# Optimization experiments

Measured on AMD Instinct MI355X. Metric: run time of the kernel, lower is better.

The kernel has to match this reference:

```python
import jax, jax.numpy as jnp
import numpy as np

B, V, D, H = 8192, 5, 1792, 14
HD = D // H  # head dim = 128
NEG = jnp.float32(-1e30)  # stand-in for -inf in the adjacency mask


def setup_inputs() -> dict:
    key = jax.random.key(0)
    ks = jax.random.split(key, 5)
    vertices = jax.random.normal(ks[0], (B, V, D), dtype=jnp.float32)
    adjacency = jax.random.randint(ks[1], (V, V), 0, 2, dtype=jnp.int32)
    # ensure no all-masked row (self connection), matching a valid pentachoron graph
    adjacency = adjacency.at[jnp.arange(V), jnp.arange(V)].set(1)
    scale = 1.0 / np.sqrt(D)
    in_proj_w = jax.random.normal(ks[2], (3 * D, D), dtype=jnp.float32) * scale
    in_proj_b = jnp.zeros((3 * D,), dtype=jnp.float32)
    out_proj_w = jax.random.normal(ks[3], (D, D), dtype=jnp.float32) * scale
    out_proj_b = jnp.zeros((D,), dtype=jnp.float32)
    return {"vertices": vertices, "adjacency": adjacency,
            "in_proj_w": in_proj_w, "in_proj_b": in_proj_b,
            "out_proj_w": out_proj_w, "out_proj_b": out_proj_b}


def reference(vertices, adjacency, in_proj_w, in_proj_b, out_proj_w, out_proj_b):
    # Fused equivalent of looping MultiheadAttention over the 5 vertices:
    # query i attends over all 5 vertices, masked by adjacency row i.
    qkv = jnp.einsum('bvd,ed->bve', vertices, in_proj_w) + in_proj_b  # [B,V,3D]
    q, k, v = jnp.split(qkv, 3, axis=-1)
    # [B,H,V,HD]
    q = q.reshape(B, V, H, HD).transpose(0, 2, 1, 3)
    k = k.reshape(B, V, H, HD).transpose(0, 2, 1, 3)
    v = v.reshape(B, V, H, HD).transpose(0, 2, 1, 3)
    scores = jnp.einsum('bhqd,bhkd->bhqk', q, k) / jnp.float32(np.sqrt(HD))
    mask = jnp.where(adjacency == 0, NEG, jnp.float32(0.0))  # [V,V]
    scores = scores + mask[None, None, :, :]
    attn = jax.nn.softmax(scores, axis=-1)
    out = jnp.einsum('bhqk,bhkd->bhqd', attn, v)  # [B,H,V,HD]
    out = out.transpose(0, 2, 1, 3).reshape(B, V, D)
    return jnp.einsum('bvd,ed->bve', out, out_proj_w) + out_proj_b
```

## Files before the change

kernel.cpp:

```cpp
#include <hip/hip_runtime.h>
#include <hip/hip_bf16.h>

#define Bsz   8192
#define Vn    5
#define Dm    1792
#define Hn    14
#define HDm   128
#define Mrows (Bsz * Vn)
#define N1    (3 * Dm)
#define Kd    Dm

typedef float f32x4 __attribute__((ext_vector_type(4)));
typedef short bf16x8 __attribute__((ext_vector_type(8)));

__device__ __forceinline__ ushort f2bf(float f) {
    unsigned u = __float_as_uint(f);
    u += 0x7fffu + ((u >> 16) & 1u);
    return (ushort)(u >> 16);
}
__device__ __forceinline__ float bf2f(ushort h) {
    return __uint_as_float(((unsigned)h) << 16);
}

#define AS1(p) ((const __attribute__((address_space(1))) void*)(p))
#define AS3(p) ((__attribute__((address_space(3))) void*)(p))

__global__ void cvt_kernel(const float* __restrict__ in, ushort* __restrict__ out, int n4) {
    int i = blockIdx.x * blockDim.x + threadIdx.x;
    int stride = gridDim.x * blockDim.x;
    for (int idx = i; idx < n4; idx += stride) {
        float4 v = reinterpret_cast<const float4*>(in)[idx];
        ushort4 o;
        o.x = f2bf(v.x); o.y = f2bf(v.y); o.z = f2bf(v.z); o.w = f2bf(v.w);
        reinterpret_cast<ushort4*>(out)[idx] = o;
    }
}

template<bool OUT_BF16>
__global__ __launch_bounds__(512, 2) void gemm8p(
    const ushort* __restrict__ A,
    const ushort* __restrict__ Bw,
    const float* __restrict__ bias,
    void* __restrict__ Cout,
    int M, int N, int K)
{
    __shared__ __align__(16) char smem[131072];

    const int nTN = N >> 8;
    int bid = blockIdx.x;
    int cpx = gridDim.x >> 3;
    int swz = (bid & 7) * cpx + (bid >> 3);
    int gsz = 4 * nTN;
    int g = swz / gsz, r = swz - g * gsz;
    int bm = g * 4 + (r & 3);
    int bn = r >> 2;

    int t = threadIdx.x;
    int lane = t & 63, w = t >> 6;
    int wrow = (w >> 2) * 128;
    int wcol = (w & 3) * 64;
    int fr = lane & 15, fq = lane >> 4;
    int slotC = ((fq ^ ((fr >> 1) & 3)) << 4);
    int aOff = (wrow + fr) * 64 + slotC;
    int bOff = 32768 + (wcol + fr) * 64 + slotC;

    size_t K2 = (size_t)K * 2;
    size_t rowSkip = (size_t)128 * K2;
    int rowL = t >> 2;
    int slotSw = (((t & 3) ^ ((t >> 3) & 3)) << 4);
    const char* aSrc = (const char*)A + (size_t)(bm * 256 + rowL) * K2 + slotSw;
    const char* bSrc = (const char*)Bw + (size_t)(bn * 256 + rowL) * K2 + slotSw;

    f32x4 acc[8][4] = {};
    bf16x8 af0[4], af1[4], bf0[4], bf1[4];

#define STAGE(SRC, UOFF, KT, KH) { \
    const char* _s = (SRC) + (size_t)(KT) * 128 + (KH) * 64; \
    __builtin_amdgcn_global_load_lds(AS1(_s), AS3(&smem[(UOFF) + t * 16]), 16, 0, 0); \
    __builtin_amdgcn_global_load_lds(AS1(_s + rowSkip), AS3(&smem[(UOFF) + 8192 + t * 16]), 16, 0, 0); }

#define RDA(DST, BUF, KS, M0) { \
    DST[0] = *(const bf16x8*)&smem[(BUF)*65536 + (KS)*16384 + ((M0)+0)*1024 + aOff]; \
    DST[1] = *(const bf16x8*)&smem[(BUF)*65536 + (KS)*16384 + ((M0)+1)*1024 + aOff]; \
    DST[2] = *(const bf16x8*)&smem[(BUF)*65536 + (KS)*16384 + ((M0)+2)*1024 + aOff]; \
    DST[3] = *(const bf16x8*)&smem[(BUF)*65536 + (KS)*16384 + ((M0)+3)*1024 + aOff]; }

#define RDB(DST, BUF, KS) { \
    DST[0] = *(const bf16x8*)&smem[(BUF)*65536 + (KS)*16384 + 0*1024 + bOff]; \
    DST[1] = *(const bf16x8*)&smem[(BUF)*65536 + (KS)*16384 + 1*1024 + bOff]; \
    DST[2] = *(const bf16x8*)&smem[(BUF)*65536 + (KS)*16384 + 2*1024 + bOff]; \
    DST[3] = *(const bf16x8*)&smem[(BUF)*65536 + (KS)*16384 + 3*1024 + bOff]; }

#define MFMAQ(AF, BF, M0) { \
    __builtin_amdgcn_s_setprio(1); \
    _Pragma("unroll") \
    for (int mi = 0; mi < 4; ++mi) { \
      _Pragma("unroll") \
      for (int ni = 0; ni < 4; ++ni) \
        acc[(M0)+mi][ni] = __builtin_amdgcn_mfma_f32_16x16x32_bf16(AF[mi], BF[ni], acc[(M0)+mi][ni], 0, 0, 0); \
    } \
    __builtin_amdgcn_s_setprio(0); }

#define BAR __builtin_amdgcn_s_barrier()
#define VMC(N) asm volatile("s_waitcnt vmcnt(" #N ")" ::: "memory")

    STAGE(aSrc, 0,      0, 0);
    STAGE(bSrc, 32768,  0, 0);
    STAGE(aSrc, 16384,  0, 1);
    STAGE(bSrc, 49152,  0, 1);
    STAGE(aSrc, 65536,  1, 0);
    STAGE(bSrc, 98304,  1, 0);
    VMC(8);
    BAR;
    RDA(af0, 0, 0, 0); RDB(bf0, 0, 0);

    const int NIT = K / 128;
    #pragma unroll 1
    for (int it = 0; it < NIT - 1; ++it) {
        int kt1 = 2 * it + 1, kt2 = 2 * it + 2, kt3 = 2 * it + 3;
        MFMAQ(af0, bf0, 0); RDA(af1, 0, 0, 4);                 STAGE(aSrc, 81920, kt1, 1);
        VMC(6); BAR;
        MFMAQ(af1, bf0, 4); RDA(af0, 0, 1, 0); RDB(bf1, 0, 1); STAGE(bSrc, 114688, kt1, 1);
        BAR;
        MFMAQ(af0, bf1, 0); RDA(af1, 0, 1, 4);                 STAGE(aSrc, 0, kt2, 0);
        VMC(6); BAR;
        MFMAQ(af1, bf1, 4); RDA(af0, 1, 0, 0); RDB(bf0, 1, 0); STAGE(bSrc, 32768, kt2, 0);
        BAR;
        MFMAQ(af0, bf0, 0); RDA(af1, 1, 0, 4);                 STAGE(aSrc, 16384, kt2, 1);
        VMC(6); BAR;
        MFMAQ(af1, bf0, 4); RDA(af0, 1, 1, 0); RDB(bf1, 1, 1); STAGE(bSrc, 49152, kt2, 1);
        BAR;
        MFMAQ(af0, bf1, 0); RDA(af1, 1, 1, 4);                 STAGE(aSrc, 65536, kt3, 0);
        VMC(6); BAR;
        MFMAQ(af1, bf1, 4); RDA(af0, 0, 0, 0); RDB(bf0, 0, 0); STAGE(bSrc, 98304, kt3, 0);
        BAR;
    }
    {
        int kt1 = 2 * NIT - 1;
        MFMAQ(af0, bf0, 0); RDA(af1, 0, 0, 4);                 STAGE(aSrc, 81920, kt1, 1);
        VMC(6); BAR;
        MFMAQ(af1, bf0, 4); RDA(af0, 0, 1, 0); RDB(bf1, 0, 1); STAGE(bSrc, 114688, kt1, 1);
        BAR;
        MFMAQ(af0, bf1, 0); RDA(af1, 0, 1, 4);
        VMC(4); BAR;
        MFMAQ(af1, bf1, 4); RDA(af0, 1, 0, 0); RDB(bf0, 1, 0);
        BAR;
        MFMAQ(af0, bf0, 0); RDA(af1, 1, 0, 4);
        VMC(0); BAR;
        MFMAQ(af1, bf0, 4); RDA(af0, 1, 1, 0); RDB(bf1, 1, 1);
        BAR;
        MFMAQ(af0, bf1, 0); RDA(af1, 1, 1, 4);
        BAR;
        MFMAQ(af1, bf1, 4);
    }

#undef STAGE
#undef RDA
#undef RDB
#undef MFMAQ
#undef BAR
#undef VMC

    float*  Cf = (float*)Cout;
    ushort* Cb = (ushort*)Cout;
    #pragma unroll
    for (int mi = 0; mi < 8; ++mi) {
        int row0 = bm * 256 + wrow + mi * 16 + fq * 4;
        #pragma unroll
        for (int ni = 0; ni < 4; ++ni) {
            int col = bn * 256 + wcol + ni * 16 + fr;
            float bv = bias[col];
            #pragma unroll
            for (int rr = 0; rr < 4; ++rr) {
                float val = acc[mi][ni][rr] + bv;
                size_t off = (size_t)(row0 + rr) * N + col;
                if (OUT_BF16) Cb[off] = f2bf(val);
                else          Cf[off] = val;
            }
        }
    }
}

__global__ __launch_bounds__(256) void attn_kernel(
    const ushort* __restrict__ qkv,
    const int* __restrict__ adj,
    ushort* __restrict__ outp)
{
    int gw = blockIdx.x * 4 + (threadIdx.x >> 6);
    int lane = threadIdx.x & 63;
    int b = gw / Hn;
    int h = gw - b * Hn;

    const ushort* base = qkv + (size_t)b * 5 * N1 + h * HDm + 2 * lane;
    float q[5][2], k[5][2], v[5][2];
    #pragma unroll
    for (int i = 0; i < 5; ++i) {
        ushort2 qq = *reinterpret_cast<const ushort2*>(base + (size_t)i * N1);
        ushort2 kk = *reinterpret_cast<const ushort2*>(base + (size_t)i * N1 + Dm);
        ushort2 vv = *reinterpret_cast<const ushort2*>(base + (size_t)i * N1 + 2 * Dm);
        q[i][0] = bf2f(qq.x); q[i][1] = bf2f(qq.y);
        k[i][0] = bf2f(kk.x); k[i][1] = bf2f(kk.y);
        v[i][0] = bf2f(vv.x); v[i][1] = bf2f(vv.y);
    }

    float s[5][5];
    #pragma unroll
    for (int i = 0; i < 5; ++i)
        #pragma unroll
        for (int j = 0; j < 5; ++j) {
            float p = q[i][0] * k[j][0] + q[i][1] * k[j][1];
            #pragma unroll
            for (int off = 32; off > 0; off >>= 1)
                p += __shfl_xor(p, off);
            s[i][j] = p;
        }

    const float scale = 0.08838834764831845f;
    float aw[5][5];
    #pragma unroll
    for (int i = 0; i < 5; ++i) {
        float sv[5];
        float mx = -3.0e38f;
        #pragma unroll
        for (int j = 0; j < 5; ++j) {
            float val = s[i][j] * scale + (adj[i * 5 + j] == 0 ? -1e30f : 0.0f);
            sv[j] = val;
            mx = fmaxf(mx, val);
        }
        float denom = 0.0f;
        #pragma unroll
        for (int j = 0; j < 5; ++j) { sv[j] = __expf(sv[j] - mx); denom += sv[j]; }
        float rd = 1.0f / denom;
        #pragma unroll
        for (int j = 0; j < 5; ++j) aw[i][j] = sv[j] * rd;
    }

    ushort* ob = outp + (size_t)b * 5 * Dm + h * HDm + 2 * lane;
    #pragma unroll
    for (int i = 0; i < 5; ++i) {
        float o0 = 0.0f, o1 = 0.0f;
        #pragma unroll
        for (int j = 0; j < 5; ++j) { o0 += aw[i][j] * v[j][0]; o1 += aw[i][j] * v[j][1]; }
        ushort2 ov; ov.x = f2bf(o0); ov.y = f2bf(o1);
        *reinterpret_cast<ushort2*>(ob + (size_t)i * Dm) = ov;
    }
}

extern "C" void kernel_launch(void* const* d_in, const int* in_sizes, int n_in,
                              void* d_out, int out_size, void* d_ws, size_t ws_size,
                              hipStream_t stream) {
    const float* vertices  = (const float*)d_in[0];
    const int*   adjacency = (const int*)  d_in[1];
    const float* w1        = (const float*)d_in[2];
    const float* b1        = (const float*)d_in[3];
    const float* w2        = (const float*)d_in[4];
    const float* b2        = (const float*)d_in[5];
    float* out = (float*)d_out;

    char* ws = (char*)d_ws;
    const size_t vertBytes = (size_t)Mrows * Kd * 2;
    const size_t qkvBytes  = (size_t)Mrows * N1 * 2;
    const size_t w1Bytes   = (size_t)N1 * Kd * 2;
    const size_t w2Bytes   = (size_t)Dm * Dm * 2;
    const size_t needed    = vertBytes + qkvBytes + w1Bytes + w2Bytes;
    if (ws_size < needed) return;

    ushort* vert_bf = (ushort*)ws;
    ushort* qkv_bf  = (ushort*)(ws + vertBytes);
    ushort* w1_bf   = (ushort*)(ws + vertBytes + qkvBytes);
    ushort* w2_bf   = (ushort*)(ws + vertBytes + qkvBytes + w1Bytes);

    cvt_kernel<<<2048, 256, 0, stream>>>(vertices, vert_bf, Mrows * Kd / 4);
    cvt_kernel<<<512,  256, 0, stream>>>(w1, w1_bf, N1 * Kd / 4);
    cvt_kernel<<<256,  256, 0, stream>>>(w2, w2_bf, Dm * Dm / 4);

    gemm8p<true><<<(Mrows / 256) * (N1 / 256), 512, 0, stream>>>(
        vert_bf, w1_bf, b1, qkv_bf, Mrows, N1, Kd);

    attn_kernel<<<Bsz * Hn / 4, 256, 0, stream>>>(qkv_bf, adjacency, vert_bf);

    gemm8p<false><<<(Mrows / 256) * (Dm / 256), 512, 0, stream>>>(
        vert_bf, w2_bf, b2, out, Mrows, Dm, Kd);
}
```

Measured before the change: 1.204 ms.

## Load GEMM B fragments directly from global into registers, halve LDS

The weight (B) operand is no longer staged through shared memory. Each lane now loads its bf16x8 B fragments straight from global memory into registers, one k-step ahead. The LDS buffer drops from 128 KB to 64 KB and holds only A tiles in a four-slot ring, with vmcnt waits retuned to match. This removes LDS traffic and footprint for B and may allow more resident blocks. In exchange, B global loads are uncoalesced per wave and latency must be hidden by the register prefetch.

```diff
diff --git a/kernel.cpp b/kernel.cpp
--- a/kernel.cpp
+++ b/kernel.cpp
@@ -44,7 +44,7 @@
     void* __restrict__ Cout,
     int M, int N, int K)
 {
-    __shared__ __align__(16) char smem[131072];
+    __shared__ __align__(16) char smem[65536];
 
     const int nTN = N >> 8;
     int bid = blockIdx.x;
@@ -62,34 +62,35 @@
     int fr = lane & 15, fq = lane >> 4;
     int slotC = ((fq ^ ((fr >> 1) & 3)) << 4);
     int aOff = (wrow + fr) * 64 + slotC;
-    int bOff = 32768 + (wcol + fr) * 64 + slotC;
 
     size_t K2 = (size_t)K * 2;
     size_t rowSkip = (size_t)128 * K2;
     int rowL = t >> 2;
     int slotSw = (((t & 3) ^ ((t >> 3) & 3)) << 4);
     const char* aSrc = (const char*)A + (size_t)(bm * 256 + rowL) * K2 + slotSw;
-    const char* bSrc = (const char*)Bw + (size_t)(bn * 256 + rowL) * K2 + slotSw;
+
+    const ushort* bB = Bw + (size_t)(bn * 256 + wcol + fr) * K + fq * 8;
 
     f32x4 acc[8][4] = {};
-    bf16x8 af0[4], af1[4], bf0[4], bf1[4];
-
-#define STAGE(SRC, UOFF, KT, KH) { \
-    const char* _s = (SRC) + (size_t)(KT) * 128 + (KH) * 64; \
+    bf16x8 af0[4], af1[4], bfA[4], bfB[4];
+
+#define STAGE(UOFF, KT, KH) { \
+    const char* _s = aSrc + (size_t)(KT) * 128 + (KH) * 64; \
     __builtin_amdgcn_global_load_lds(AS1(_s), AS3(&smem[(UOFF) + t * 16]), 16, 0, 0); \
     __builtin_amdgcn_global_load_lds(AS1(_s + rowSkip), AS3(&smem[(UOFF) + 8192 + t * 16]), 16, 0, 0); }
 
-#define RDA(DST, BUF, KS, M0) { \
-    DST[0] = *(const bf16x8*)&smem[(BUF)*65536 + (KS)*16384 + ((M0)+0)*1024 + aOff]; \
-    DST[1] = *(const bf16x8*)&smem[(BUF)*65536 + (KS)*16384 + ((M0)+1)*1024 + aOff]; \
-    DST[2] = *(const bf16x8*)&smem[(BUF)*65536 + (KS)*16384 + ((M0)+2)*1024 + aOff]; \
-    DST[3] = *(const bf16x8*)&smem[(BUF)*65536 + (KS)*16384 + ((M0)+3)*1024 + aOff]; }
-
-#define RDB(DST, BUF, KS) { \
-    DST[0] = *(const bf16x8*)&smem[(BUF)*65536 + (KS)*16384 + 0*1024 + bOff]; \
-    DST[1] = *(const bf16x8*)&smem[(BUF)*65536 + (KS)*16384 + 1*1024 + bOff]; \
-    DST[2] = *(const bf16x8*)&smem[(BUF)*65536 + (KS)*16384 + 2*1024 + bOff]; \
-    DST[3] = *(const bf16x8*)&smem[(BUF)*65536 + (KS)*16384 + 3*1024 + bOff]; }
+#define RDA(DST, UOFF, M0) { \
+    DST[0] = *(const bf16x8*)&smem[(UOFF) + ((M0)+0)*1024 + aOff]; \
+    DST[1] = *(const bf16x8*)&smem[(UOFF) + ((M0)+1)*1024 + aOff]; \
+    DST[2] = *(const bf16x8*)&smem[(UOFF) + ((M0)+2)*1024 + aOff]; \
+    DST[3] = *(const bf16x8*)&smem[(UOFF) + ((M0)+3)*1024 + aOff]; }
+
+#define LDB(DST, KT, KS) { \
+    const ushort* _b = bB + (size_t)(KT) * 64 + (KS) * 32; \
+    DST[0] = *(const bf16x8*)(_b); \
+    DST[1] = *(const bf16x8*)(_b + (size_t)16 * K); \
+    DST[2] = *(const bf16x8*)(_b + (size_t)32 * K); \
+    DST[3] = *(const bf16x8*)(_b + (size_t)48 * K); }
 
 #define MFMAQ(AF, BF, M0) { \
     __builtin_amdgcn_s_setprio(1); \
@@ -102,63 +103,71 @@
     __builtin_amdgcn_s_setprio(0); }
 
 #define BAR __builtin_amdgcn_s_barrier()
+#define SBR __builtin_amdgcn_sched_barrier(0)
 #define VMC(N) asm volatile("s_waitcnt vmcnt(" #N ")" ::: "memory")
 
-    STAGE(aSrc, 0,      0, 0);
-    STAGE(bSrc, 32768,  0, 0);
-    STAGE(aSrc, 16384,  0, 1);
-    STAGE(bSrc, 49152,  0, 1);
-    STAGE(aSrc, 65536,  1, 0);
-    STAGE(bSrc, 98304,  1, 0);
+    STAGE(0,     0, 0);
+    STAGE(16384, 0, 1);
+    STAGE(32768, 1, 0);
+    SBR;
+    LDB(bfA, 0, 0);
     VMC(8);
     BAR;
-    RDA(af0, 0, 0, 0); RDB(bf0, 0, 0);
+    RDA(af0, 0, 0);
 
     const int NIT = K / 128;
     #pragma unroll 1
     for (int it = 0; it < NIT - 1; ++it) {
-        int kt1 = 2 * it + 1, kt2 = 2 * it + 2, kt3 = 2 * it + 3;
-        MFMAQ(af0, bf0, 0); RDA(af1, 0, 0, 4);                 STAGE(aSrc, 81920, kt1, 1);
-        VMC(6); BAR;
-        MFMAQ(af1, bf0, 4); RDA(af0, 0, 1, 0); RDB(bf1, 0, 1); STAGE(bSrc, 114688, kt1, 1);
-        BAR;
-        MFMAQ(af0, bf1, 0); RDA(af1, 0, 1, 4);                 STAGE(aSrc, 0, kt2, 0);
-        VMC(6); BAR;
-        MFMAQ(af1, bf1, 4); RDA(af0, 1, 0, 0); RDB(bf0, 1, 0); STAGE(bSrc, 32768, kt2, 0);
-        BAR;
-        MFMAQ(af0, bf0, 0); RDA(af1, 1, 0, 4);                 STAGE(aSrc, 16384, kt2, 1);
-        VMC(6); BAR;
-        MFMAQ(af1, bf0, 4); RDA(af0, 1, 1, 0); RDB(bf1, 1, 1); STAGE(bSrc, 49152, kt2, 1);
-        BAR;
-        MFMAQ(af0, bf1, 0); RDA(af1, 1, 1, 4);                 STAGE(aSrc, 65536, kt3, 0);
-        VMC(6); BAR;
-        MFMAQ(af1, bf1, 4); RDA(af0, 0, 0, 0); RDB(bf0, 0, 0); STAGE(bSrc, 98304, kt3, 0);
+        int T0 = 2 * it, kt1 = T0 + 1, kt2 = T0 + 2, kt3 = T0 + 3;
+        MFMAQ(af0, bfA, 0); RDA(af1, 0, 4);
+        STAGE(49152, kt1, 1); SBR; LDB(bfB, T0, 1);
+        BAR;
+        MFMAQ(af1, bfA, 4); VMC(12); RDA(af0, 16384, 0);
+        BAR;
+        MFMAQ(af0, bfB, 0); RDA(af1, 16384, 4);
+        STAGE(0, kt2, 0); SBR; LDB(bfA, kt1, 0);
+        BAR;
+        MFMAQ(af1, bfB, 4); VMC(16); RDA(af0, 32768, 0);
+        BAR;
+        MFMAQ(af0, bfA, 0); RDA(af1, 32768, 4);
+        STAGE(16384, kt2, 1); SBR; LDB(bfB, kt1, 1);
+        BAR;
+        MFMAQ(af1, bfA, 4); VMC(16); RDA(af0, 49152, 0);
+        BAR;
+        MFMAQ(af0, bfB, 0); RDA(af1, 49152, 4);
+        STAGE(32768, kt3, 0); SBR; LDB(bfA, kt2, 0);
+        BAR;
+        MFMAQ(af1, bfB, 4); VMC(16); RDA(af0, 0, 0);
         BAR;
     }
     {
-        int kt1 = 2 * NIT - 1;
-        MFMAQ(af0, bf0, 0); RDA(af1, 0, 0, 4);                 STAGE(aSrc, 81920, kt1, 1);
-        VMC(6); BAR;
-        MFMAQ(af1, bf0, 4); RDA(af0, 0, 1, 0); RDB(bf1, 0, 1); STAGE(bSrc, 114688, kt1, 1);
-        BAR;
-        MFMAQ(af0, bf1, 0); RDA(af1, 0, 1, 4);
-        VMC(4); BAR;
-        MFMAQ(af1, bf1, 4); RDA(af0, 1, 0, 0); RDB(bf0, 1, 0);
-        BAR;
-        MFMAQ(af0, bf0, 0); RDA(af1, 1, 0, 4);
-        VMC(0); BAR;
-        MFMAQ(af1, bf0, 4); RDA(af0, 1, 1, 0); RDB(bf1, 1, 1);
-        BAR;
-        MFMAQ(af0, bf1, 0); RDA(af1, 1, 1, 4);
-        BAR;
-        MFMAQ(af1, bf1, 4);
+        int T0 = 2 * NIT - 2, kt1 = T0 + 1;
+        MFMAQ(af0, bfA, 0); RDA(af1, 0, 4);
+        STAGE(49152, kt1, 1); SBR; LDB(bfB, T0, 1);
+        BAR;
+        MFMAQ(af1, bfA, 4); VMC(12); RDA(af0, 16384, 0);
+        BAR;
+        MFMAQ(af0, bfB, 0); RDA(af1, 16384, 4);
+        SBR; LDB(bfA, kt1, 0);
+        BAR;
+        MFMAQ(af1, bfB, 4); VMC(10); RDA(af0, 32768, 0);
+        BAR;
+        MFMAQ(af0, bfA, 0); RDA(af1, 32768, 4);
+        SBR; LDB(bfB, kt1, 1);
+        BAR;
+        MFMAQ(af1, bfA, 4); VMC(8); RDA(af0, 49152, 0);
+        BAR;
+        MFMAQ(af0, bfB, 0); RDA(af1, 49152, 4);
+        BAR;
+        MFMAQ(af1, bfB, 4);
     }
 
 #undef STAGE
 #undef RDA
-#undef RDB
+#undef LDB
 #undef MFMAQ
 #undef BAR
+#undef SBR
 #undef VMC
 
     float*  Cf = (float*)Cout;
```

After: 1.495 ms. 1.24x slower.
